# Optimization experiments

Hardware: AMD Instinct MI355X
Metric: run time of the kernel (lower is better)

The kernel has to match this reference:

```python
import jax, jax.numpy as jnp
import numpy as np

E = 1024   # embed_dim
H = 16     # num_heads
R = 256    # rank
HD = E // H
B, S = 2, 2048


def setup_inputs() -> dict:
    key = jax.random.key(0)
    ks = jax.random.split(key, 20)
    sc = 0.02
    d = {
        'query': jax.random.normal(ks[0], (B, S, E), jnp.float32),
        'key':   jax.random.normal(ks[1], (B, S, E), jnp.float32),
        'value': jax.random.normal(ks[2], (B, S, E), jnp.float32),
    }
    names = ['q', 'k', 'v', 'o']
    i = 3
    for n in names:
        d[f'W{n}_lo'] = jax.random.normal(ks[i], (E, R), jnp.float32) * sc; i += 1
        d[f'b{n}_lo'] = jnp.zeros((R,), jnp.float32)
        d[f'W{n}_hi'] = jax.random.normal(ks[i], (R, E), jnp.float32) * sc; i += 1
        d[f'b{n}_hi'] = jnp.zeros((E,), jnp.float32)
    return d


def _lowrank(x, W_lo, b_lo, W_hi, b_hi):
    # Linear(E->R) then Linear(R->E)
    return (x @ W_lo + b_lo) @ W_hi + b_hi


def reference(query, key, value,
              Wq_lo, bq_lo, Wq_hi, bq_hi,
              Wk_lo, bk_lo, Wk_hi, bk_hi,
              Wv_lo, bv_lo, Wv_hi, bv_hi,
              Wo_lo, bo_lo, Wo_hi, bo_hi):
    b, s, _ = query.shape
    q = _lowrank(query, Wq_lo, bq_lo, Wq_hi, bq_hi)
    k = _lowrank(key,   Wk_lo, bk_lo, Wk_hi, bk_hi)
    v = _lowrank(value, Wv_lo, bv_lo, Wv_hi, bv_hi)
    # (B, S, E) -> (B, H, S, HD)
    q = q.reshape(b, s, H, HD).transpose(0, 2, 1, 3)
    k = k.reshape(b, s, H, HD).transpose(0, 2, 1, 3)
    v = v.reshape(b, s, H, HD).transpose(0, 2, 1, 3)
    scores = jnp.einsum('bhqd,bhkd->bhqk', q, k) / jnp.sqrt(jnp.float32(HD))
    attn = jax.nn.softmax(scores, axis=-1)  # dropout p=0.0 -> identity
    out = jnp.einsum('bhqk,bhkd->bhqd', attn, v)
    out = out.transpose(0, 2, 1, 3).reshape(b, s, E)
    return _lowrank(out, Wo_lo, bo_lo, Wo_hi, bo_hi)
```

## Files before the change

kernel.cpp:

```cpp
#include <hip/hip_runtime.h>

namespace {

constexpr int kE  = 1024;
constexpr int kH  = 16;
constexpr int kR  = 256;
constexpr int kHD = 64;
constexpr int kB  = 2;
constexpr int kS  = 2048;
constexpr int kM  = kB * kS;

typedef float  floatx4 __attribute__((ext_vector_type(4)));
typedef short  short8  __attribute__((ext_vector_type(8)));
typedef short  short4  __attribute__((ext_vector_type(4)));

__device__ inline short f2bf(float f) {
  union { float f; unsigned u; } x{f};
  unsigned r = x.u + 0x7FFF + ((x.u >> 16) & 1);
  return (short)(r >> 16);
}

__device__ inline void async_copy16(const void* g, void* l) {
  __builtin_amdgcn_global_load_lds(
      (const __attribute__((address_space(1))) unsigned int*)g,
      (__attribute__((address_space(3))) unsigned int*)l,
      16, 0, 0);
}

#if defined(__HIP_DEVICE_COMPILE__)
  #if __has_builtin(__builtin_amdgcn_mfma_f32_16x16x16bf16_1k)
    #define MFMA16(a, b, c) __builtin_amdgcn_mfma_f32_16x16x16bf16_1k(a, b, c, 0, 0, 0)
  #elif __has_builtin(__builtin_amdgcn_mfma_f32_16x16x16_bf16)
    #define MFMA16(a, b, c) __builtin_amdgcn_mfma_f32_16x16x16_bf16(a, b, c, 0, 0, 0)
  #else
    #error "no 16x16x16 bf16 MFMA builtin on device"
  #endif
#else
  #define MFMA16(a, b, c) (c)
#endif

struct PrepArgs { const float* src[8]; short* dst[8]; };

__global__ __launch_bounds__(256) void prep_weights(PrepArgs pa) {
  const int id = blockIdx.y;
  const bool lo = (id & 1) == 0;
  const int K = lo ? 1024 : 256;
  const int N = lo ? 256 : 1024;
  const int tiles_k = K >> 6;
  const int k0 = (blockIdx.x % tiles_k) * 64;
  const int n0 = (blockIdx.x / tiles_k) * 64;
  const float* src = pa.src[id];
  short* dst = pa.dst[id];

  __shared__ float tile[64][68];
  const int t  = threadIdx.x;
  const int c4 = (t & 15) * 4;
  const int r  = t >> 4;

#pragma unroll
  for (int i = 0; i < 4; ++i) {
    const int rk = r + i * 16;
    *(float4*)&tile[rk][c4] = *(const float4*)&src[(size_t)(k0 + rk) * N + n0 + c4];
  }
  __syncthreads();
#pragma unroll
  for (int i = 0; i < 4; ++i) {
    const int rn = r + i * 16;
    short4 o = { f2bf(tile[c4 + 0][rn]), f2bf(tile[c4 + 1][rn]),
                 f2bf(tile[c4 + 2][rn]), f2bf(tile[c4 + 3][rn]) };
    *(short4*)&dst[(size_t)(n0 + rn) * K + k0 + c4] = o;
  }
}

__global__ __launch_bounds__(256) void convert_in(
    const float* q, const float* k, const float* v,
    short* xq, short* xk, short* xv)
{
  const float* srcs[3] = {q, k, v};
  short* dsts[3] = {xq, xk, xv};
  const float* s = srcs[blockIdx.y];
  short* d = dsts[blockIdx.y];
  const size_t i = ((size_t)blockIdx.x * 256 + threadIdx.x) * 8;
  float4 a = *(const float4*)(s + i);
  float4 b = *(const float4*)(s + i + 4);
  short8 o = { f2bf(a.x), f2bf(a.y), f2bf(a.z), f2bf(a.w),
               f2bf(b.x), f2bf(b.y), f2bf(b.z), f2bf(b.w) };
  *(short8*)(d + i) = o;
}

struct GemmArgs {
  const short* A[3]; const short* Bt[3]; const float* bias[3];
  void* C[3]; float scale[3];
};

template <int N, int K, int BM, int BN, int MODE>
__global__ __launch_bounds__(256) void gemm_bf16(GemmArgs args) {
  constexpr int TILES_N = N / BN;
  constexpr int WTM = BM / 2, WTN = BN / 2;
  constexpr int FI = WTM / 16, FJ = WTN / 16;
  constexpr int AROUNDS = (BM * 64) / 4096;
  constexpr int BROUNDS = (BN * 64) / 4096;

  const int z = blockIdx.y;
  const int row0 = (blockIdx.x / TILES_N) * BM;
  const int col0 = (blockIdx.x % TILES_N) * BN;
  const short* A  = args.A[z];
  const short* Bt = args.Bt[z];
  const float* bias = args.bias[z];
  const float scale = args.scale[z];

  __shared__ short As[BM * 32];
  __shared__ short Bs[BN * 32];

  const int t    = threadIdx.x;
  const int wave = t >> 6;
  const int lane = t & 63;
  const int lq   = lane & 15;
  const int quad = lane >> 4;
  const int wm0  = (wave >> 1) * WTM;
  const int wn0  = (wave & 1) * WTN;

  const int srow = t >> 2;
  const int scol = (t & 3) * 8;

  floatx4 acc[FI][FJ] = {};

  for (int kk = 0; kk < K; kk += 32) {
#pragma unroll
    for (int r = 0; r < AROUNDS; ++r)
      async_copy16(A + (size_t)(row0 + r * 64 + srow) * K + kk + scol,
                   (char*)As + r * 4096 + wave * 1024);
#pragma unroll
    for (int r = 0; r < BROUNDS; ++r)
      async_copy16(Bt + (size_t)(col0 + r * 64 + srow) * K + kk + scol,
                   (char*)Bs + r * 4096 + wave * 1024);
    __syncthreads();

    short8 af[FI], bf[FJ];
#pragma unroll
    for (int i = 0; i < FI; ++i)
      af[i] = *(const short8*)((const char*)As + ((wm0 + i * 16 + lq) * 64 + quad * 16));
#pragma unroll
    for (int j = 0; j < FJ; ++j)
      bf[j] = *(const short8*)((const char*)Bs + ((wn0 + j * 16 + lq) * 64 + quad * 16));
#pragma unroll
    for (int i = 0; i < FI; ++i)
#pragma unroll
      for (int j = 0; j < FJ; ++j)
        acc[i][j] = __builtin_amdgcn_mfma_f32_16x16x32_bf16(af[i], bf[j], acc[i][j], 0, 0, 0);
    __syncthreads();
  }

#pragma unroll
  for (int i = 0; i < FI; ++i) {
    const int rbase = row0 + wm0 + i * 16 + quad * 4;
#pragma unroll
    for (int j = 0; j < FJ; ++j) {
      const int col = col0 + wn0 + j * 16 + lq;
      const float bj = bias[col];
      if (MODE == 2) {
        float* C = (float*)args.C[z];
#pragma unroll
        for (int r = 0; r < 4; ++r)
          C[(size_t)(rbase + r) * N + col] = (acc[i][j][r] + bj) * scale;
      } else if (MODE == 1) {
        short* C = (short*)args.C[z];
        const int h = col >> 6, d = col & 63;
        const int b = rbase >> 11, s = rbase & 2047;
        if (z == 2) {
          short4 o = { f2bf(acc[i][j][0] + bj), f2bf(acc[i][j][1] + bj),
                       f2bf(acc[i][j][2] + bj), f2bf(acc[i][j][3] + bj) };
          *(short4*)&C[((size_t)((b * 16 + h) * 64 + d)) * 2048 + s] = o;
        } else {
#pragma unroll
          for (int r = 0; r < 4; ++r)
            C[((size_t)((b * 16 + h) * 2048 + s + r)) * 64 + d] =
                f2bf((acc[i][j][r] + bj) * scale);
        }
      } else {
        short* C = (short*)args.C[z];
#pragma unroll
        for (int r = 0; r < 4; ++r)
          C[(size_t)(rbase + r) * N + col] = f2bf((acc[i][j][r] + bj) * scale);
      }
    }
  }
}

__global__ __launch_bounds__(256) void attn_mfma(
    const short* __restrict__ Qp, const short* __restrict__ Kp,
    const short* __restrict__ Vtp, short* __restrict__ O)
{
  __shared__ short Ks[64][72];
  __shared__ short Vs[64][72];

  const int t    = threadIdx.x;
  const int wave = t >> 6;
  const int lane = t & 63;
  const int lq   = lane & 15;
  const int quad = lane >> 4;

  const int q0 = blockIdx.x * 64;
  const int bh = blockIdx.y;
  const int b  = bh >> 4;
  const int h  = bh & 15;

  const short* qrow = Qp + ((size_t)bh * kS + q0 + wave * 16 + lq) * 64;
  short8 qf0 = *(const short8*)(qrow + quad * 8);
  short8 qf1 = *(const short8*)(qrow + 32 + quad * 8);

  const short* Kbase = Kp  + (size_t)bh * kS * 64;
  const short* Vbase = Vtp + (size_t)bh * 64 * kS;

  const int srow = wave * 16 + (lane >> 3);
  const int scol = (lane & 7) * 8;

  floatx4 Oacc[4] = {};
  float m = -1e30f;
  float l = 0.f;

  short8 gk0 = *(const short8*)(Kbase + (size_t)(srow) * 64 + scol);
  short8 gk1 = *(const short8*)(Kbase + (size_t)(srow + 8) * 64 + scol);
  short8 gv0 = *(const short8*)(Vbase + (size_t)srow * kS + scol);
  short8 gv1 = *(const short8*)(Vbase + (size_t)(srow + 8) * kS + scol);

  for (int kc = 0; kc < kS; kc += 64) {
    __syncthreads();
    *(short8*)&Ks[srow][scol]     = gk0;
    *(short8*)&Ks[srow + 8][scol] = gk1;
    *(short8*)&Vs[srow][scol]     = gv0;
    *(short8*)&Vs[srow + 8][scol] = gv1;
    __syncthreads();

    if (kc + 64 < kS) {
      gk0 = *(const short8*)(Kbase + (size_t)(kc + 64 + srow) * 64 + scol);
      gk1 = *(const short8*)(Kbase + (size_t)(kc + 64 + srow + 8) * 64 + scol);
      gv0 = *(const short8*)(Vbase + (size_t)srow * kS + kc + 64 + scol);
      gv1 = *(const short8*)(Vbase + (size_t)(srow + 8) * kS + kc + 64 + scol);
    }

    floatx4 Sc[4];
#pragma unroll
    for (int tt = 0; tt < 4; ++tt) {
      short8 a0 = *(const short8*)&Ks[tt * 16 + lq][quad * 8];
      short8 a1 = *(const short8*)&Ks[tt * 16 + lq][32 + quad * 8];
      floatx4 c = {};
      c = __builtin_amdgcn_mfma_f32_16x16x32_bf16(a0, qf0, c, 0, 0, 0);
      c = __builtin_amdgcn_mfma_f32_16x16x32_bf16(a1, qf1, c, 0, 0, 0);
      Sc[tt] = c;
    }

    float mc = -1e30f;
#pragma unroll
    for (int tt = 0; tt < 4; ++tt)
#pragma unroll
      for (int r = 0; r < 4; ++r) mc = fmaxf(mc, Sc[tt][r]);
    mc = fmaxf(mc, __shfl_xor(mc, 16, 64));
    mc = fmaxf(mc, __shfl_xor(mc, 32, 64));
    const float mn = fmaxf(m, mc);
    const float alpha = __expf(m - mn);
    m = mn;

    float ls = 0.f;
    short4 pf[4];
#pragma unroll
    for (int tt = 0; tt < 4; ++tt) {
      float p0 = __expf(Sc[tt][0] - m);
      float p1 = __expf(Sc[tt][1] - m);
      float p2 = __expf(Sc[tt][2] - m);
      float p3 = __expf(Sc[tt][3] - m);
      ls += (p0 + p1) + (p2 + p3);
      pf[tt] = short4{ f2bf(p0), f2bf(p1), f2bf(p2), f2bf(p3) };
    }
    l = l * alpha + ls;
#pragma unroll
    for (int dt = 0; dt < 4; ++dt)
#pragma unroll
      for (int r = 0; r < 4; ++r) Oacc[dt][r] *= alpha;

#pragma unroll
    for (int dt = 0; dt < 4; ++dt) {
#pragma unroll
      for (int tt = 0; tt < 4; ++tt) {
        short4 vf = *(const short4*)&Vs[dt * 16 + lq][tt * 16 + quad * 4];
        Oacc[dt] = MFMA16(vf, pf[tt], Oacc[dt]);
      }
    }
  }

  l += __shfl_xor(l, 16, 64);
  l += __shfl_xor(l, 32, 64);
  const float inv = 1.f / l;

  short* orow = O + ((size_t)(b * kS + q0 + wave * 16 + lq)) * kE + h * kHD;
#pragma unroll
  for (int dt = 0; dt < 4; ++dt) {
    short4 o = { f2bf(Oacc[dt][0] * inv), f2bf(Oacc[dt][1] * inv),
                 f2bf(Oacc[dt][2] * inv), f2bf(Oacc[dt][3] * inv) };
    *(short4*)&orow[dt * 16 + quad * 4] = o;
  }
}

}

extern "C" void kernel_launch(void* const* d_in, const int* in_sizes, int n_in,
                              void* d_out, int out_size, void* d_ws, size_t ws_size,
                              hipStream_t stream) {
  short* ws = (short*)d_ws;
  short* Xq  = ws;
  short* Xk  = Xq  + (size_t)kM * kE;
  short* Xv  = Xk  + (size_t)kM * kE;
  short* Tq  = Xv  + (size_t)kM * kE;
  short* Tk  = Tq  + (size_t)kM * kR;
  short* Tv  = Tk  + (size_t)kM * kR;
  short* Qh  = Tv  + (size_t)kM * kR;
  short* Kh  = Qh  + (size_t)kM * kE;
  short* Vth = Kh  + (size_t)kM * kE;
  short* Ab  = Vth + (size_t)kM * kE;
  short* To  = Ab  + (size_t)kM * kE;
  short* Wt  = To  + (size_t)kM * kR;

  short* WtArr[8];
  for (int i = 0; i < 8; ++i) WtArr[i] = Wt + (size_t)i * (kE * kR);

  PrepArgs pa;
  const int widx[8] = {3, 5, 7, 9, 11, 13, 15, 17};
  for (int i = 0; i < 8; ++i) { pa.src[i] = (const float*)d_in[widx[i]]; pa.dst[i] = WtArr[i]; }
  prep_weights<<<dim3(64, 8), dim3(256), 0, stream>>>(pa);

  convert_in<<<dim3((kM * kE) / (256 * 8), 3), dim3(256), 0, stream>>>(
      (const float*)d_in[0], (const float*)d_in[1], (const float*)d_in[2], Xq, Xk, Xv);

  {
    GemmArgs ga;
    ga.A[0] = Xq; ga.A[1] = Xk; ga.A[2] = Xv;
    ga.Bt[0] = WtArr[0]; ga.Bt[1] = WtArr[2]; ga.Bt[2] = WtArr[4];
    ga.bias[0] = (const float*)d_in[4]; ga.bias[1] = (const float*)d_in[8]; ga.bias[2] = (const float*)d_in[12];
    ga.C[0] = Tq; ga.C[1] = Tk; ga.C[2] = Tv;
    ga.scale[0] = ga.scale[1] = ga.scale[2] = 1.f;
    gemm_bf16<kR, kE, 64, 64, 0><<<dim3((kM / 64) * (kR / 64), 3), dim3(256), 0, stream>>>(ga);
  }

  {
    GemmArgs ga;
    ga.A[0] = Tq; ga.A[1] = Tk; ga.A[2] = Tv;
    ga.Bt[0] = WtArr[1]; ga.Bt[1] = WtArr[3]; ga.Bt[2] = WtArr[5];
    ga.bias[0] = (const float*)d_in[6]; ga.bias[1] = (const float*)d_in[10]; ga.bias[2] = (const float*)d_in[14];
    ga.C[0] = Qh; ga.C[1] = Kh; ga.C[2] = Vth;
    ga.scale[0] = 0.125f; ga.scale[1] = 1.f; ga.scale[2] = 1.f;
    gemm_bf16<kE, kR, 128, 128, 1><<<dim3((kM / 128) * (kE / 128), 3), dim3(256), 0, stream>>>(ga);
  }

  attn_mfma<<<dim3(kS / 64, kB * kH), dim3(256), 0, stream>>>(Qh, Kh, Vth, Ab);

  {
    GemmArgs ga;
    ga.A[0] = Ab; ga.Bt[0] = WtArr[6];
    ga.bias[0] = (const float*)d_in[16];
    ga.C[0] = To; ga.scale[0] = 1.f;
    gemm_bf16<kR, kE, 64, 64, 0><<<dim3((kM / 64) * (kR / 64), 1), dim3(256), 0, stream>>>(ga);
  }
  {
    GemmArgs ga;
    ga.A[0] = To; ga.Bt[0] = WtArr[7];
    ga.bias[0] = (const float*)d_in[18];
    ga.C[0] = d_out; ga.scale[0] = 1.f;
    gemm_bf16<kE, kR, 128, 128, 2><<<dim3((kM / 128) * (kE / 128), 1), dim3(256), 0, stream>>>(ga);
  }
}
```

Before: 261.9 us.

## Compose low-rank weight pairs into dense matrices and fold log2e into Q scale

Each call now multiplies W_lo by W_hi to build a dense E×E weight per projection and folds b_lo through W_hi into a combined bias. Each projection then runs as a single E×E GEMM, which drops the rank-R intermediate buffers and two of the GEMM launches. The cost is roughly twice the projection FLOPs plus an extra composition GEMM and a small bias kernel. Separately, log2(e) is folded into the Q scale so softmax can use exp2f, and bf16 packing uses a byte-permute with round-half-up instead of round-to-nearest-even.

```diff
diff --git a/kernel.cpp b/kernel.cpp
--- a/kernel.cpp
+++ b/kernel.cpp
@@ -18,6 +18,23 @@
   union { float f; unsigned u; } x{f};
   unsigned r = x.u + 0x7FFF + ((x.u >> 16) & 1);
   return (short)(r >> 16);
+}
+
+__device__ inline unsigned pack2bf(float a, float b) {
+#if defined(__HIP_DEVICE_COMPILE__)
+  unsigned ua = __float_as_uint(a) + 0x8000u;
+  unsigned ub = __float_as_uint(b) + 0x8000u;
+  return __builtin_amdgcn_perm(ub, ua, 0x07060302u);
+#else
+  (void)a; (void)b; return 0;
+#endif
+}
+
+__device__ inline short4 pack4bf(float p0, float p1, float p2, float p3) {
+  union { unsigned u[2]; short4 s; } r;
+  r.u[0] = pack2bf(p0, p1);
+  r.u[1] = pack2bf(p2, p3);
+  return r.s;
 }
 
 __device__ inline void async_copy16(const void* g, void* l) {
@@ -39,16 +56,12 @@
   #define MFMA16(a, b, c) (c)
 #endif
 
-struct PrepArgs { const float* src[8]; short* dst[8]; };
-
-__global__ __launch_bounds__(256) void prep_weights(PrepArgs pa) {
+struct Prep4 { const float* src[4]; short* dst[4]; };
+
+__global__ __launch_bounds__(256) void prep_hi(Prep4 pa) {
   const int id = blockIdx.y;
-  const bool lo = (id & 1) == 0;
-  const int K = lo ? 1024 : 256;
-  const int N = lo ? 256 : 1024;
-  const int tiles_k = K >> 6;
-  const int k0 = (blockIdx.x % tiles_k) * 64;
-  const int n0 = (blockIdx.x / tiles_k) * 64;
+  const int k0 = (blockIdx.x & 3) * 64;
+  const int n0 = (blockIdx.x >> 2) * 64;
   const float* src = pa.src[id];
   short* dst = pa.dst[id];
 
@@ -60,7 +73,7 @@
 #pragma unroll
   for (int i = 0; i < 4; ++i) {
     const int rk = r + i * 16;
-    *(float4*)&tile[rk][c4] = *(const float4*)&src[(size_t)(k0 + rk) * N + n0 + c4];
+    *(float4*)&tile[rk][c4] = *(const float4*)&src[(size_t)(k0 + rk) * kE + n0 + c4];
   }
   __syncthreads();
 #pragma unroll
@@ -68,8 +81,31 @@
     const int rn = r + i * 16;
     short4 o = { f2bf(tile[c4 + 0][rn]), f2bf(tile[c4 + 1][rn]),
                  f2bf(tile[c4 + 2][rn]), f2bf(tile[c4 + 3][rn]) };
-    *(short4*)&dst[(size_t)(n0 + rn) * K + k0 + c4] = o;
-  }
+    *(short4*)&dst[(size_t)(n0 + rn) * kR + k0 + c4] = o;
+  }
+}
+
+__global__ __launch_bounds__(256) void prep_lo(Prep4 pa) {
+  const float* s = pa.src[blockIdx.y];
+  short* d = pa.dst[blockIdx.y];
+  const size_t i = ((size_t)blockIdx.x * 256 + threadIdx.x) * 8;
+  float4 a = *(const float4*)(s + i);
+  float4 b = *(const float4*)(s + i + 4);
+  short8 o = { f2bf(a.x), f2bf(a.y), f2bf(a.z), f2bf(a.w),
+               f2bf(b.x), f2bf(b.y), f2bf(b.z), f2bf(b.w) };
+  *(short8*)(d + i) = o;
+}
+
+struct BiasArgs { const float* blo[4]; const float* whi[4]; const float* bhi[4]; float* bc[4]; };
+
+__global__ __launch_bounds__(256) void bias_compose(BiasArgs ba) {
+  const int m = blockIdx.y;
+  const int col = blockIdx.x * 256 + threadIdx.x;
+  const float* blo = ba.blo[m];
+  const float* whi = ba.whi[m];
+  float acc = ba.bhi[m][col];
+  for (int r = 0; r < kR; ++r) acc += blo[r] * whi[(size_t)r * kE + col];
+  ba.bc[m][col] = acc;
 }
 
 __global__ __launch_bounds__(256) void convert_in(
@@ -89,8 +125,8 @@
 }
 
 struct GemmArgs {
-  const short* A[3]; const short* Bt[3]; const float* bias[3];
-  void* C[3]; float scale[3];
+  const short* A[4]; const short* Bt[4]; const float* bias[4];
+  void* C[4]; float scale[4];
 };
 
 template <int N, int K, int BM, int BN, int MODE>
@@ -157,7 +193,7 @@
 #pragma unroll
     for (int j = 0; j < FJ; ++j) {
       const int col = col0 + wn0 + j * 16 + lq;
-      const float bj = bias[col];
+      const float bj = (MODE == 3) ? 0.f : bias[col];
       if (MODE == 2) {
         float* C = (float*)args.C[z];
 #pragma unroll
@@ -168,8 +204,8 @@
         const int h = col >> 6, d = col & 63;
         const int b = rbase >> 11, s = rbase & 2047;
         if (z == 2) {
-          short4 o = { f2bf(acc[i][j][0] + bj), f2bf(acc[i][j][1] + bj),
-                       f2bf(acc[i][j][2] + bj), f2bf(acc[i][j][3] + bj) };
+          short4 o = pack4bf(acc[i][j][0] + bj, acc[i][j][1] + bj,
+                             acc[i][j][2] + bj, acc[i][j][3] + bj);
           *(short4*)&C[((size_t)((b * 16 + h) * 64 + d)) * 2048 + s] = o;
         } else {
 #pragma unroll
@@ -258,19 +294,19 @@
     mc = fmaxf(mc, __shfl_xor(mc, 16, 64));
     mc = fmaxf(mc, __shfl_xor(mc, 32, 64));
     const float mn = fmaxf(m, mc);
-    const float alpha = __expf(m - mn);
+    const float alpha = exp2f(m - mn);
     m = mn;
 
     float ls = 0.f;
     short4 pf[4];
 #pragma unroll
     for (int tt = 0; tt < 4; ++tt) {
-      float p0 = __expf(Sc[tt][0] - m);
-      float p1 = __expf(Sc[tt][1] - m);
-      float p2 = __expf(Sc[tt][2] - m);
-      float p3 = __expf(Sc[tt][3] - m);
+      float p0 = exp2f(Sc[tt][0] - m);
+      float p1 = exp2f(Sc[tt][1] - m);
+      float p2 = exp2f(Sc[tt][2] - m);
+      float p3 = exp2f(Sc[tt][3] - m);
       ls += (p0 + p1) + (p2 + p3);
-      pf[tt] = short4{ f2bf(p0), f2bf(p1), f2bf(p2), f2bf(p3) };
+      pf[tt] = pack4bf(p0, p1, p2, p3);
     }
     l = l * alpha + ls;
 #pragma unroll
@@ -295,8 +331,8 @@
   short* orow = O + ((size_t)(b * kS + q0 + wave * 16 + lq)) * kE + h * kHD;
 #pragma unroll
   for (int dt = 0; dt < 4; ++dt) {
-    short4 o = { f2bf(Oacc[dt][0] * inv), f2bf(Oacc[dt][1] * inv),
-                 f2bf(Oacc[dt][2] * inv), f2bf(Oacc[dt][3] * inv) };
+    short4 o = pack4bf(Oacc[dt][0] * inv, Oacc[dt][1] * inv,
+                       Oacc[dt][2] * inv, Oacc[dt][3] * inv);
     *(short4*)&orow[dt * 16 + quad * 4] = o;
   }
 }
@@ -307,64 +343,87 @@
                               void* d_out, int out_size, void* d_ws, size_t ws_size,
                               hipStream_t stream) {
   short* ws = (short*)d_ws;
-  short* Xq  = ws;
-  short* Xk  = Xq  + (size_t)kM * kE;
-  short* Xv  = Xk  + (size_t)kM * kE;
-  short* Tq  = Xv  + (size_t)kM * kE;
-  short* Tk  = Tq  + (size_t)kM * kR;
-  short* Tv  = Tk  + (size_t)kM * kR;
-  short* Qh  = Tv  + (size_t)kM * kR;
-  short* Kh  = Qh  + (size_t)kM * kE;
-  short* Vth = Kh  + (size_t)kM * kE;
-  short* Ab  = Vth + (size_t)kM * kE;
-  short* To  = Ab  + (size_t)kM * kE;
-  short* Wt  = To  + (size_t)kM * kR;
-
-  short* WtArr[8];
-  for (int i = 0; i < 8; ++i) WtArr[i] = Wt + (size_t)i * (kE * kR);
-
-  PrepArgs pa;
-  const int widx[8] = {3, 5, 7, 9, 11, 13, 15, 17};
-  for (int i = 0; i < 8; ++i) { pa.src[i] = (const float*)d_in[widx[i]]; pa.dst[i] = WtArr[i]; }
-  prep_weights<<<dim3(64, 8), dim3(256), 0, stream>>>(pa);
+  short* Xq   = ws;
+  short* Xk   = Xq   + (size_t)kM * kE;
+  short* Xv   = Xk   + (size_t)kM * kE;
+  short* Qh   = Xv   + (size_t)kM * kE;
+  short* Kh   = Qh   + (size_t)kM * kE;
+  short* Vth  = Kh   + (size_t)kM * kE;
+  short* Ab   = Vth  + (size_t)kM * kE;
+  short* WhiT = Ab   + (size_t)kM * kE;
+  short* WloB = WhiT + (size_t)4 * kE * kR;
+  short* WcT  = WloB + (size_t)4 * kE * kR;
+  float* bc   = (float*)(WcT + (size_t)4 * kE * kE);
+
+  short* WhiTArr[4], *WloBArr[4], *WcTArr[4];
+  float* bcArr[4];
+  for (int i = 0; i < 4; ++i) {
+    WhiTArr[i] = WhiT + (size_t)i * kE * kR;
+    WloBArr[i] = WloB + (size_t)i * kE * kR;
+    WcTArr[i]  = WcT  + (size_t)i * kE * kE;
+    bcArr[i]   = bc + i * kE;
+  }
+
+  constexpr float kQScale = 0.125f * 1.44269504088896341f;
+
+  const int wlo_i[4] = {3, 7, 11, 15};
+  const int blo_i[4] = {4, 8, 12, 16};
+  const int whi_i[4] = {5, 9, 13, 17};
+  const int bhi_i[4] = {6, 10, 14, 18};
+
+  {
+    Prep4 ph, pl;
+    for (int i = 0; i < 4; ++i) {
+      ph.src[i] = (const float*)d_in[whi_i[i]]; ph.dst[i] = WhiTArr[i];
+      pl.src[i] = (const float*)d_in[wlo_i[i]]; pl.dst[i] = WloBArr[i];
+    }
+    prep_hi<<<dim3(64, 4), dim3(256), 0, stream>>>(ph);
+    prep_lo<<<dim3((kE * kR) / (256 * 8), 4), dim3(256), 0, stream>>>(pl);
+  }
+
+  {
+    BiasArgs ba;
+    for (int i = 0; i < 4; ++i) {
+      ba.blo[i] = (const float*)d_in[blo_i[i]];
+      ba.whi[i] = (const float*)d_in[whi_i[i]];
+      ba.bhi[i] = (const float*)d_in[bhi_i[i]];
+      ba.bc[i]  = bcArr[i];
+    }
+    bias_compose<<<dim3(kE / 256, 4), dim3(256), 0, stream>>>(ba);
+  }
 
   convert_in<<<dim3((kM * kE) / (256 * 8), 3), dim3(256), 0, stream>>>(
       (const float*)d_in[0], (const float*)d_in[1], (const float*)d_in[2], Xq, Xk, Xv);
 
   {
-    GemmArgs ga;
+    GemmArgs ga = {};
+    for (int i = 0; i < 4; ++i) {
+      ga.A[i] = WhiTArr[i]; ga.Bt[i] = WloBArr[i];
+      ga.C[i] = WcTArr[i];  ga.scale[i] = 1.f;
+    }
+    gemm_bf16<kE, kR, 128, 128, 3>
+        <<<dim3((kE / 128) * (kE / 128), 4), dim3(256), 0, stream>>>(ga);
+  }
+
+  {
+    GemmArgs ga = {};
     ga.A[0] = Xq; ga.A[1] = Xk; ga.A[2] = Xv;
-    ga.Bt[0] = WtArr[0]; ga.Bt[1] = WtArr[2]; ga.Bt[2] = WtArr[4];
-    ga.bias[0] = (const float*)d_in[4]; ga.bias[1] = (const float*)d_in[8]; ga.bias[2] = (const float*)d_in[12];
-    ga.C[0] = Tq; ga.C[1] = Tk; ga.C[2] = Tv;
-    ga.scale[0] = ga.scale[1] = ga.scale[2] = 1.f;
-    gemm_bf16<kR, kE, 64, 64, 0><<<dim3((kM / 64) * (kR / 64), 3), dim3(256), 0, stream>>>(ga);
-  }
+    ga.Bt[0] = WcTArr[0]; ga.Bt[1] = WcTArr[1]; ga.Bt[2] = WcTArr[2];
+    ga.bias[0] = bcArr[0]; ga.bias[1] = bcArr[1]; ga.bias[2] = bcArr[2];
+    ga.C[0] = Qh; ga.C[1] = Kh; ga.C[2] = Vth;
+    ga.scale[0] = kQScale; ga.scale[1] = 1.f; ga.scale[2] = 1.f;
+    gemm_bf16<kE, kE, 128, 128, 1>
+        <<<dim3((kM / 128) * (kE / 128), 3), dim3(256), 0, stream>>>(ga);
+  }
+
+  attn_mfma<<<dim3(kS / 64, kB * kH), dim3(256), 0, stream>>>(Qh, Kh, Vth, Ab);
 
   {
-    GemmArgs ga;
-    ga.A[0] = Tq; ga.A[1] = Tk; ga.A[2] = Tv;
-    ga.Bt[0] = WtArr[1]; ga.Bt[1] = WtArr[3]; ga.Bt[2] = WtArr[5];
-    ga.bias[0] = (const float*)d_in[6]; ga.bias[1] = (const float*)d_in[10]; ga.bias[2] = (const float*)d_in[14];
-    ga.C[0] = Qh; ga.C[1] = Kh; ga.C[2] = Vth;
-    ga.scale[0] = 0.125f; ga.scale[1] = 1.f; ga.scale[2] = 1.f;
-    gemm_bf16<kE, kR, 128, 128, 1><<<dim3((kM / 128) * (kE / 128), 3), dim3(256), 0, stream>>>(ga);
-  }
-
-  attn_mfma<<<dim3(kS / 64, kB * kH), dim3(256), 0, stream>>>(Qh, Kh, Vth, Ab);
-
-  {
-    GemmArgs ga;
-    ga.A[0] = Ab; ga.Bt[0] = WtArr[6];
-    ga.bias[0] = (const float*)d_in[16];
-    ga.C[0] = To; ga.scale[0] = 1.f;
-    gemm_bf16<kR, kE, 64, 64, 0><<<dim3((kM / 64) * (kR / 64), 1), dim3(256), 0, stream>>>(ga);
-  }
-  {
-    GemmArgs ga;
-    ga.A[0] = To; ga.Bt[0] = WtArr[7];
-    ga.bias[0] = (const float*)d_in[18];
+    GemmArgs ga = {};
+    ga.A[0] = Ab; ga.Bt[0] = WcTArr[3];
+    ga.bias[0] = bcArr[3];
     ga.C[0] = d_out; ga.scale[0] = 1.f;
-    gemm_bf16<kE, kR, 128, 128, 2><<<dim3((kM / 128) * (kE / 128), 1), dim3(256), 0, stream>>>(ga);
-  }
-}
+    gemm_bf16<kE, kE, 128, 128, 2>
+        <<<dim3((kM / 128) * (kE / 128), 1), dim3(256), 0, stream>>>(ga);
+  }
+}
```

Result: slower. 292.7 us (+11.8%).
